# Optimization experiments

Measured on AMD Instinct MI355X. Metric: run time of the kernel, lower is better.

The kernel has to match this reference:

```python
import jax, jax.numpy as jnp
import numpy as np

B, N, C_IN, C_CH = 1, 512, 128, 128

def layer_norm(x, g, b, eps=1e-5):
    mu = jnp.mean(x, axis=-1, keepdims=True)
    var = jnp.var(x, axis=-1, keepdims=True)
    return (x - mu) * jax.lax.rsqrt(var + eps) * g + b

def setup_inputs() -> dict:
    key = jax.random.key(0)
    ks = jax.random.split(key, 16)
    s = 0.02
    # weights stored as [in, out] (torch Linear uses y = x @ W.T + b; we pre-transpose)
    return {
        "z": jax.random.normal(ks[0], (B, N, N, C_IN), jnp.float32),
        "mask": jax.random.randint(ks[1], (B, N, N), 0, 2).astype(bool),
        "g_in": jnp.ones((C_IN,), jnp.float32),
        "b_in": jnp.zeros((C_IN,), jnp.float32),
        "Wa": jax.random.normal(ks[2], (C_IN, C_CH), jnp.float32) * s,
        "ba": jnp.zeros((C_CH,), jnp.float32),
        "Wga": jax.random.normal(ks[3], (C_IN, C_CH), jnp.float32) * s,
        "bga": jax.random.normal(ks[4], (C_CH,), jnp.float32) * s,
        "Wb": jax.random.normal(ks[5], (C_IN, C_CH), jnp.float32) * s,
        "bb": jnp.zeros((C_CH,), jnp.float32),
        "Wgb": jax.random.normal(ks[6], (C_IN, C_CH), jnp.float32) * s,
        "bgb": jax.random.normal(ks[7], (C_CH,), jnp.float32) * s,
        "g_o": jnp.ones((C_CH,), jnp.float32),
        "b_o": jnp.zeros((C_CH,), jnp.float32),
        "Wgo": jax.random.normal(ks[8], (C_IN, C_IN), jnp.float32) * s,
        "bgo": jax.random.normal(ks[9], (C_IN,), jnp.float32) * s,
        "Wo": jax.random.normal(ks[10], (C_CH, C_IN), jnp.float32) * s,
        "bo": jnp.zeros((C_IN,), jnp.float32),
    }

def reference(z, mask, g_in, b_in, Wa, ba, Wga, bga, Wb, bb, Wgb, bgb,
              g_o, b_o, Wgo, bgo, Wo, bo):
    zn = layer_norm(z, g_in, b_in)                                  # [B,N,N,Cin]
    a = jax.nn.sigmoid(zn @ Wga + bga) * (zn @ Wa + ba)             # [B,N,N,Cch]
    b = jax.nn.sigmoid(zn @ Wgb + bgb) * (zn @ Wb + bb)
    m = mask[..., None]                                             # [B,N,N,1]
    a = jnp.where(m, 0.0, a)
    b = jnp.where(m, 0.0, b)
    # axis == 1: k[b,i,j,o] = sum_k a[b,i,k,o] * b[b,j,k,o]
    k = jnp.einsum('biko,bjko->bijo', a, b)
    return jax.nn.sigmoid(zn @ Wgo + bgo) * (layer_norm(k, g_o, b_o) @ Wo + bo)
```

## Files before the change

### kernel.cpp

```cpp
#include <hip/hip_runtime.h>

#define NDIM 512
#define CDIM 128
#define RDIM (NDIM * NDIM)

typedef __attribute__((ext_vector_type(8))) short bf16x8;
typedef __attribute__((ext_vector_type(8))) unsigned short ushort8;
typedef __attribute__((ext_vector_type(4))) float f32x4;

__device__ __forceinline__ float bf2f(unsigned short u) {
  union { unsigned int i; float f; } v; v.i = ((unsigned int)u) << 16; return v.f;
}
__device__ __forceinline__ unsigned short f2bf(float f) {
  union { float f; unsigned int i; } v; v.f = f;
  unsigned int r = v.i + 0x7fffu + ((v.i >> 16) & 1u);
  return (unsigned short)(r >> 16);
}
__device__ __forceinline__ float sigm(float x) { return 1.0f / (1.0f + __expf(-x)); }

__device__ __forceinline__ int sw(int row, int col) {
  return (row << 7) + ((((col >> 3) ^ (row & 7)) << 3) | (col & 7));
}

__global__ __launch_bounds__(256) void k0_prep(
    const float* __restrict__ Wga, const float* __restrict__ Wa,
    const float* __restrict__ Wgb, const float* __restrict__ Wb,
    const float* __restrict__ Wgo, const float* __restrict__ Wo,
    unsigned short* __restrict__ wsT, unsigned short* __restrict__ wsF) {
  __shared__ unsigned short T[128 * 130];
  const float* src;
  switch (blockIdx.x) {
    case 0: src = Wga; break;
    case 1: src = Wa;  break;
    case 2: src = Wgb; break;
    case 3: src = Wb;  break;
    case 4: src = Wgo; break;
    default: src = Wo; break;
  }
  const int t = threadIdx.x;
  unsigned short* dstT = wsT + blockIdx.x * (CDIM * CDIM);
  const int r = t >> 1, hf = t & 1;
  const float* s = src + r * CDIM + hf * 64;
  for (int i = 0; i < 64; i++) T[r * 130 + hf * 64 + i] = f2bf(s[i]);
  __syncthreads();
  unsigned short* d = dstT + r * CDIM + hf * 64;
  for (int i = 0; i < 64; i++) d[i] = T[(hf * 64 + i) * 130 + r];
  unsigned short* dstF = wsF + blockIdx.x * 16384;
  for (int gid = t; gid < 2048; gid += 256) {
    const int fragid = gid >> 6, lane = gid & 63;
    const int kc = fragid >> 3, nf = fragid & 7;
    const int o = nf * 16 + (lane & 15);
    const int c0 = kc * 32 + (lane >> 4) * 8;
#pragma unroll
    for (int j = 0; j < 8; j++) dstF[gid * 8 + j] = f2bf(src[(c0 + j) * CDIM + o]);
  }
}

__device__ __forceinline__ bf16x8 ldfrag(const unsigned short* wf, int slot, int kc,
                                         int nf, int lane) {
  return *((const bf16x8*)(wf + (((slot * 32 + kc * 8 + nf) * 64 + lane) << 3)));
}

__global__ __launch_bounds__(256, 3) void k1_proj(
    const float* __restrict__ z, const int* __restrict__ mask,
    const float* __restrict__ g_in, const float* __restrict__ b_in,
    const float* __restrict__ bga, const float* __restrict__ ba,
    const float* __restrict__ bgb, const float* __restrict__ bb,
    const float* __restrict__ bgo, const unsigned short* __restrict__ wf,
    unsigned short* __restrict__ a_t, unsigned short* __restrict__ b_t,
    float* __restrict__ gate_out) {
  __shared__ unsigned short Xs[CDIM * CDIM];
  const int t = threadIdx.x;
  const int lane = t & 63;
  const int w = t >> 6;
  const int l15 = lane & 15, lq = lane >> 4;
  const int row0 = blockIdx.x * 128;

  {
    const int row = t >> 1, hf = t & 1;
    const float4* zp = (const float4*)(z + (size_t)(row0 + row) * CDIM + hf * 64);
    float s = 0.f, s2 = 0.f;
#pragma unroll
    for (int i = 0; i < 16; i++) {
      float4 x = zp[i];
      s += x.x + x.y + x.z + x.w;
      s2 += x.x * x.x + x.y * x.y + x.z * x.z + x.w * x.w;
    }
    s += __shfl_xor(s, 1);
    s2 += __shfl_xor(s2, 1);
    const float mean = s * 0.0078125f;
    const float var = s2 * 0.0078125f - mean * mean;
    const float rs = rsqrtf(var + 1e-5f);
    const float4* gp = (const float4*)(g_in + hf * 64);
    const float4* bp = (const float4*)(b_in + hf * 64);
#pragma unroll 4
    for (int u = 0; u < 8; u++) {
      float4 x0 = zp[2 * u], x1 = zp[2 * u + 1];
      float4 g0 = gp[2 * u], g1 = gp[2 * u + 1];
      float4 c0 = bp[2 * u], c1 = bp[2 * u + 1];
      ushort8 pk;
      pk[0] = f2bf((x0.x - mean) * rs * g0.x + c0.x);
      pk[1] = f2bf((x0.y - mean) * rs * g0.y + c0.y);
      pk[2] = f2bf((x0.z - mean) * rs * g0.z + c0.z);
      pk[3] = f2bf((x0.w - mean) * rs * g0.w + c0.w);
      pk[4] = f2bf((x1.x - mean) * rs * g1.x + c1.x);
      pk[5] = f2bf((x1.y - mean) * rs * g1.y + c1.y);
      pk[6] = f2bf((x1.z - mean) * rs * g1.z + c1.z);
      pk[7] = f2bf((x1.w - mean) * rs * g1.w + c1.w);
      const int su = (hf * 8 + u) ^ (row & 7);
      *((ushort8*)&Xs[(row << 7) + (su << 3)]) = pk;
    }
  }

  unsigned mbits = 0;
#pragma unroll
  for (int ms = 0; ms < 2; ms++)
#pragma unroll
    for (int r = 0; r < 4; r++) {
      const int rl = w * 32 + ms * 16 + (lq << 2) + r;
      if (mask[row0 + rl] != 0) mbits |= 1u << (ms * 4 + r);
    }

  __syncthreads();

  bf16x8 afr[2][4];
#pragma unroll
  for (int ms = 0; ms < 2; ms++) {
    const int m = w * 32 + ms * 16 + l15;
#pragma unroll
    for (int kc = 0; kc < 4; kc++)
      afr[ms][kc] = *((const bf16x8*)&Xs[sw(m, kc * 32 + (lq << 3))]);
  }
  __syncthreads();

  const f32x4 zv = {0.f, 0.f, 0.f, 0.f};

#pragma unroll 1
  for (int pair = 0; pair < 2; pair++) {
    const int sg = pair * 2, sv = pair * 2 + 1;
    const float* bgp = (pair == 0) ? bga : bgb;
    const float* bvp = (pair == 0) ? ba : bb;
#pragma unroll 1
    for (int half = 0; half < 2; half++) {
      f32x4 accg[2][4], accv[2][4];
#pragma unroll
      for (int i = 0; i < 2; i++)
#pragma unroll
        for (int j = 0; j < 4; j++) { accg[i][j] = zv; accv[i][j] = zv; }
#pragma unroll
      for (int kc = 0; kc < 4; kc++) {
#pragma unroll
        for (int nfh = 0; nfh < 4; nfh++) {
          const int fi = half * 4 + nfh;
          bf16x8 bg = ldfrag(wf, sg, kc, fi, lane);
          bf16x8 bv = ldfrag(wf, sv, kc, fi, lane);
          accg[0][nfh] = __builtin_amdgcn_mfma_f32_16x16x32_bf16(afr[0][kc], bg, accg[0][nfh], 0, 0, 0);
          accg[1][nfh] = __builtin_amdgcn_mfma_f32_16x16x32_bf16(afr[1][kc], bg, accg[1][nfh], 0, 0, 0);
          accv[0][nfh] = __builtin_amdgcn_mfma_f32_16x16x32_bf16(afr[0][kc], bv, accv[0][nfh], 0, 0, 0);
          accv[1][nfh] = __builtin_amdgcn_mfma_f32_16x16x32_bf16(afr[1][kc], bv, accv[1][nfh], 0, 0, 0);
        }
      }
#pragma unroll
      for (int ms = 0; ms < 2; ms++)
#pragma unroll
        for (int nfh = 0; nfh < 4; nfh++) {
          const int n = half * 64 + nfh * 16 + l15;
          const float bg = bgp[n], bv = bvp[n];
#pragma unroll
          for (int r = 0; r < 4; r++) {
            const int rl = w * 32 + ms * 16 + (lq << 2) + r;
            float val = sigm(accg[ms][nfh][r] + bg) * (accv[ms][nfh][r] + bv);
            if ((mbits >> (ms * 4 + r)) & 1u) val = 0.f;
            Xs[sw(n, rl)] = f2bf(val);
          }
        }
    }
    __syncthreads();
    unsigned short* dst = (pair == 0) ? a_t : b_t;
    {
      const int o = t >> 1, hf = t & 1;
#pragma unroll
      for (int u = 0; u < 8; u++) {
        const int ru = hf * 8 + u;
        const int su = ru ^ (o & 7);
        uint4 val = *((const uint4*)&Xs[(o << 7) + (su << 3)]);
        *((uint4*)&dst[(size_t)o * RDIM + row0 + ru * 8]) = val;
      }
    }
    __syncthreads();
  }

#pragma unroll 1
  for (int half = 0; half < 2; half++) {
    f32x4 accg[2][4];
#pragma unroll
    for (int i = 0; i < 2; i++)
#pragma unroll
      for (int j = 0; j < 4; j++) accg[i][j] = zv;
#pragma unroll
    for (int kc = 0; kc < 4; kc++) {
#pragma unroll
      for (int nfh = 0; nfh < 4; nfh++) {
        bf16x8 bg = ldfrag(wf, 4, kc, half * 4 + nfh, lane);
        accg[0][nfh] = __builtin_amdgcn_mfma_f32_16x16x32_bf16(afr[0][kc], bg, accg[0][nfh], 0, 0, 0);
        accg[1][nfh] = __builtin_amdgcn_mfma_f32_16x16x32_bf16(afr[1][kc], bg, accg[1][nfh], 0, 0, 0);
      }
    }
#pragma unroll
    for (int ms = 0; ms < 2; ms++)
#pragma unroll
      for (int nfh = 0; nfh < 4; nfh++) {
        const int n = half * 64 + nfh * 16 + l15;
        const float bg = bgo[n];
#pragma unroll
        for (int r = 0; r < 4; r++) {
          const int rl = w * 32 + ms * 16 + (lq << 2) + r;
          gate_out[(size_t)(row0 + rl) * CDIM + n] = sigm(accg[ms][nfh][r] + bg);
        }
      }
  }
}

__global__ __launch_bounds__(256) void k2_einsum(
    const unsigned short* __restrict__ a_t, const unsigned short* __restrict__ b_t,
    unsigned short* __restrict__ k_t) {
  __shared__ unsigned short As[128 * 72];
  __shared__ unsigned short Bs[128 * 72];
  const int t = threadIdx.x;
  const int lane = t & 63;
  const int w = t >> 6;
  const int l15 = lane & 15, lq = lane >> 4;
  const int o = blockIdx.x >> 4;
  const int tile = blockIdx.x & 15;
  const int i0 = (tile >> 2) * 128, j0 = (tile & 3) * 128;
  const size_t base = (size_t)o * RDIM;

  f32x4 acc[2][8];
  const f32x4 zv = {0.f, 0.f, 0.f, 0.f};
#pragma unroll
  for (int i = 0; i < 2; i++)
#pragma unroll
    for (int j = 0; j < 8; j++) acc[i][j] = zv;

  const int r = t & 127;
  const int isB = t >> 7;
  const unsigned short* srcp = (isB ? b_t : a_t) + base + (size_t)((isB ? j0 : i0) + r) * NDIM;
  unsigned short* dstp = isB ? &Bs[r * 72] : &As[r * 72];

  for (int k0 = 0; k0 < NDIM; k0 += 64) {
    __syncthreads();
    const uint4* s4 = (const uint4*)(srcp + k0);
#pragma unroll
    for (int u = 0; u < 8; u++) *((uint4*)&dstp[u * 8]) = s4[u];
    __syncthreads();
#pragma unroll
    for (int kc = 0; kc < 2; kc++) {
      const int kk = kc * 32 + (lq << 3);
      bf16x8 a0 = *((const bf16x8*)&As[(w * 32 + l15) * 72 + kk]);
      bf16x8 a1 = *((const bf16x8*)&As[(w * 32 + 16 + l15) * 72 + kk]);
#pragma unroll
      for (int nf = 0; nf < 8; nf++) {
        bf16x8 bfr = *((const bf16x8*)&Bs[(nf * 16 + l15) * 72 + kk]);
        acc[0][nf] = __builtin_amdgcn_mfma_f32_16x16x32_bf16(a0, bfr, acc[0][nf], 0, 0, 0);
        acc[1][nf] = __builtin_amdgcn_mfma_f32_16x16x32_bf16(a1, bfr, acc[1][nf], 0, 0, 0);
      }
    }
  }
#pragma unroll
  for (int ms = 0; ms < 2; ms++)
#pragma unroll
    for (int nf = 0; nf < 8; nf++)
#pragma unroll
      for (int r2 = 0; r2 < 4; r2++) {
        const int mi = i0 + w * 32 + ms * 16 + (lq << 2) + r2;
        const int nj = j0 + nf * 16 + l15;
        k_t[base + (size_t)mi * NDIM + nj] = f2bf(acc[ms][nf][r2]);
      }
}

__global__ __launch_bounds__(256) void k3_final(
    const unsigned short* __restrict__ k_t, const unsigned short* __restrict__ wsW,
    const float* __restrict__ g_o, const float* __restrict__ b_o,
    const float* __restrict__ bo, float* __restrict__ out) {
  __shared__ unsigned short Ks[CDIM * CDIM];
  __shared__ unsigned short XN[CDIM * CDIM];
  const int t = threadIdx.x;
  const int lane = t & 63;
  const int w = t >> 6;
  const int l15 = lane & 15, lq = lane >> 4;
  const int row0 = blockIdx.x * 128;

  {
    const int o = t >> 1, hf = t & 1;
    const uint4* src = (const uint4*)(k_t + (size_t)o * RDIM + row0 + hf * 64);
#pragma unroll
    for (int u = 0; u < 8; u++) {
      const int ru = hf * 8 + u;
      const int su = ru ^ (o & 7);
      *((uint4*)&Ks[(o << 7) + (su << 3)]) = src[u];
    }
  }
  __syncthreads();
  {
    const int row = t >> 1, hf = t & 1;
    float x[64];
    float s = 0.f, s2 = 0.f;
#pragma unroll
    for (int i = 0; i < 64; i++) {
      x[i] = bf2f(Ks[sw(hf * 64 + i, row)]);
      s += x[i];
      s2 += x[i] * x[i];
    }
    s += __shfl_xor(s, 1);
    s2 += __shfl_xor(s2, 1);
    const float mean = s * 0.0078125f;
    const float var = s2 * 0.0078125f - mean * mean;
    const float rs = rsqrtf(var + 1e-5f);
#pragma unroll
    for (int i = 0; i < 64; i++) {
      const int o = hf * 64 + i;
      XN[sw(row, o)] = f2bf((x[i] - mean) * rs * g_o[o] + b_o[o]);
    }
  }
  __syncthreads();
  {
    const unsigned short* Wg = wsW + 5 * (CDIM * CDIM);
    const int o = t >> 1, hf = t & 1;
    const uint4* src = (const uint4*)(Wg + o * CDIM + hf * 64);
#pragma unroll
    for (int u = 0; u < 8; u++) {
      const int su = (hf * 8 + u) ^ (o & 7);
      *((uint4*)&Ks[(o << 7) + (su << 3)]) = src[u];
    }
  }
  __syncthreads();

  f32x4 acc[2][8];
  const f32x4 zv = {0.f, 0.f, 0.f, 0.f};
#pragma unroll
  for (int i = 0; i < 2; i++)
#pragma unroll
    for (int j = 0; j < 8; j++) acc[i][j] = zv;

  bf16x8 afr[2][4];
#pragma unroll
  for (int ms = 0; ms < 2; ms++) {
    const int m = w * 32 + ms * 16 + l15;
#pragma unroll
    for (int kc = 0; kc < 4; kc++)
      afr[ms][kc] = *((const bf16x8*)&XN[sw(m, kc * 32 + (lq << 3))]);
  }
#pragma unroll
  for (int kc = 0; kc < 4; kc++) {
    const int kk = kc * 32 + (lq << 3);
#pragma unroll
    for (int nf = 0; nf < 8; nf++) {
      bf16x8 bfr = *((const bf16x8*)&Ks[sw(nf * 16 + l15, kk)]);
      acc[0][nf] = __builtin_amdgcn_mfma_f32_16x16x32_bf16(afr[0][kc], bfr, acc[0][nf], 0, 0, 0);
      acc[1][nf] = __builtin_amdgcn_mfma_f32_16x16x32_bf16(afr[1][kc], bfr, acc[1][nf], 0, 0, 0);
    }
  }
#pragma unroll
  for (int ms = 0; ms < 2; ms++)
#pragma unroll
    for (int nf = 0; nf < 8; nf++) {
      const int n = nf * 16 + l15;
      const float bn = bo[n];
#pragma unroll
      for (int r = 0; r < 4; r++) {
        const int rl = w * 32 + ms * 16 + (lq << 2) + r;
        const size_t idx = (size_t)(row0 + rl) * CDIM + n;
        out[idx] = out[idx] * (acc[ms][nf][r] + bn);
      }
    }
}

extern "C" void kernel_launch(void* const* d_in, const int* in_sizes, int n_in,
                              void* d_out, int out_size, void* d_ws, size_t ws_size,
                              hipStream_t stream) {
  const float* z    = (const float*)d_in[0];
  const int*   mask = (const int*)d_in[1];
  const float* g_in = (const float*)d_in[2];
  const float* b_in = (const float*)d_in[3];
  const float* Wa   = (const float*)d_in[4];
  const float* ba   = (const float*)d_in[5];
  const float* Wga  = (const float*)d_in[6];
  const float* bga  = (const float*)d_in[7];
  const float* Wb   = (const float*)d_in[8];
  const float* bb   = (const float*)d_in[9];
  const float* Wgb  = (const float*)d_in[10];
  const float* bgb  = (const float*)d_in[11];
  const float* g_o  = (const float*)d_in[12];
  const float* b_o  = (const float*)d_in[13];
  const float* Wgo  = (const float*)d_in[14];
  const float* bgo  = (const float*)d_in[15];
  const float* Wo   = (const float*)d_in[16];
  const float* bo   = (const float*)d_in[17];
  float* out = (float*)d_out;

  unsigned short* wsT = (unsigned short*)d_ws;
  unsigned short* wsF = wsT + 6 * (CDIM * CDIM);
  unsigned short* a_t = wsF + 6 * (CDIM * CDIM);
  unsigned short* b_t = a_t + (size_t)CDIM * RDIM;
  unsigned short* k_t = b_t + (size_t)CDIM * RDIM;

  k0_prep<<<6, 256, 0, stream>>>(Wga, Wa, Wgb, Wb, Wgo, Wo, wsT, wsF);
  k1_proj<<<RDIM / 128, 256, 0, stream>>>(z, mask, g_in, b_in, bga, ba, bgb, bb,
                                          bgo, wsF, a_t, b_t, out);
  k2_einsum<<<CDIM * 16, 256, 0, stream>>>(a_t, b_t, k_t);
  k3_final<<<RDIM / 128, 256, 0, stream>>>(k_t, wsT, g_o, b_o, bo, out);
}
```

Measured before the change: 673.8 us.

## Move output gate projection into final kernel and remix einsum block order

The sigmoid(zn@Wgo) gate is no longer computed in the projection kernel and written as fp32 to the output buffer. The final kernel now recomputes the input layernorm from z and computes the gate and Wo projections together from pre-fragmented weights, writing the output once. This drops the transposed weight copy and the fp32 read-modify-write of the output. The cost is re-reading z (128 MB fp32) in the final kernel. The einsum block index is also permuted to interleave channels across blocks, and the final kernel gets a launch_bounds occupancy hint.

```diff
diff --git a/kernel.cpp b/kernel.cpp
--- a/kernel.cpp
+++ b/kernel.cpp
@@ -26,8 +26,7 @@
     const float* __restrict__ Wga, const float* __restrict__ Wa,
     const float* __restrict__ Wgb, const float* __restrict__ Wb,
     const float* __restrict__ Wgo, const float* __restrict__ Wo,
-    unsigned short* __restrict__ wsT, unsigned short* __restrict__ wsF) {
-  __shared__ unsigned short T[128 * 130];
+    unsigned short* __restrict__ wsF) {
   const float* src;
   switch (blockIdx.x) {
     case 0: src = Wga; break;
@@ -38,13 +37,6 @@
     default: src = Wo; break;
   }
   const int t = threadIdx.x;
-  unsigned short* dstT = wsT + blockIdx.x * (CDIM * CDIM);
-  const int r = t >> 1, hf = t & 1;
-  const float* s = src + r * CDIM + hf * 64;
-  for (int i = 0; i < 64; i++) T[r * 130 + hf * 64 + i] = f2bf(s[i]);
-  __syncthreads();
-  unsigned short* d = dstT + r * CDIM + hf * 64;
-  for (int i = 0; i < 64; i++) d[i] = T[(hf * 64 + i) * 130 + r];
   unsigned short* dstF = wsF + blockIdx.x * 16384;
   for (int gid = t; gid < 2048; gid += 256) {
     const int fragid = gid >> 6, lane = gid & 63;
@@ -66,9 +58,8 @@
     const float* __restrict__ g_in, const float* __restrict__ b_in,
     const float* __restrict__ bga, const float* __restrict__ ba,
     const float* __restrict__ bgb, const float* __restrict__ bb,
-    const float* __restrict__ bgo, const unsigned short* __restrict__ wf,
-    unsigned short* __restrict__ a_t, unsigned short* __restrict__ b_t,
-    float* __restrict__ gate_out) {
+    const unsigned short* __restrict__ wf,
+    unsigned short* __restrict__ a_t, unsigned short* __restrict__ b_t) {
   __shared__ unsigned short Xs[CDIM * CDIM];
   const int t = threadIdx.x;
   const int lane = t & 63;
@@ -189,36 +180,6 @@
     }
     __syncthreads();
   }
-
-#pragma unroll 1
-  for (int half = 0; half < 2; half++) {
-    f32x4 accg[2][4];
-#pragma unroll
-    for (int i = 0; i < 2; i++)
-#pragma unroll
-      for (int j = 0; j < 4; j++) accg[i][j] = zv;
-#pragma unroll
-    for (int kc = 0; kc < 4; kc++) {
-#pragma unroll
-      for (int nfh = 0; nfh < 4; nfh++) {
-        bf16x8 bg = ldfrag(wf, 4, kc, half * 4 + nfh, lane);
-        accg[0][nfh] = __builtin_amdgcn_mfma_f32_16x16x32_bf16(afr[0][kc], bg, accg[0][nfh], 0, 0, 0);
-        accg[1][nfh] = __builtin_amdgcn_mfma_f32_16x16x32_bf16(afr[1][kc], bg, accg[1][nfh], 0, 0, 0);
-      }
-    }
-#pragma unroll
-    for (int ms = 0; ms < 2; ms++)
-#pragma unroll
-      for (int nfh = 0; nfh < 4; nfh++) {
-        const int n = half * 64 + nfh * 16 + l15;
-        const float bg = bgo[n];
-#pragma unroll
-        for (int r = 0; r < 4; r++) {
-          const int rl = w * 32 + ms * 16 + (lq << 2) + r;
-          gate_out[(size_t)(row0 + rl) * CDIM + n] = sigm(accg[ms][nfh][r] + bg);
-        }
-      }
-  }
 }
 
 __global__ __launch_bounds__(256) void k2_einsum(
@@ -230,8 +191,9 @@
   const int lane = t & 63;
   const int w = t >> 6;
   const int l15 = lane & 15, lq = lane >> 4;
-  const int o = blockIdx.x >> 4;
-  const int tile = blockIdx.x & 15;
+  const int bid = (blockIdx.x & 7) * (2048 >> 3) + (blockIdx.x >> 3);
+  const int o = bid >> 4;
+  const int tile = bid & 15;
   const int i0 = (tile >> 2) * 128, j0 = (tile & 3) * 128;
   const size_t base = (size_t)o * RDIM;
 
@@ -278,9 +240,11 @@
       }
 }
 
-__global__ __launch_bounds__(256) void k3_final(
-    const unsigned short* __restrict__ k_t, const unsigned short* __restrict__ wsW,
-    const float* __restrict__ g_o, const float* __restrict__ b_o,
+__global__ __launch_bounds__(256, 2) void k3_final(
+    const unsigned short* __restrict__ k_t, const unsigned short* __restrict__ wf,
+    const float* __restrict__ z, const float* __restrict__ g_in,
+    const float* __restrict__ b_in, const float* __restrict__ g_o,
+    const float* __restrict__ b_o, const float* __restrict__ bgo,
     const float* __restrict__ bo, float* __restrict__ out) {
   __shared__ unsigned short Ks[CDIM * CDIM];
   __shared__ unsigned short XN[CDIM * CDIM];
@@ -300,22 +264,68 @@
       *((uint4*)&Ks[(o << 7) + (su << 3)]) = src[u];
     }
   }
-  __syncthreads();
   {
     const int row = t >> 1, hf = t & 1;
-    float x[64];
+    const float4* zp = (const float4*)(z + (size_t)(row0 + row) * CDIM + hf * 64);
     float s = 0.f, s2 = 0.f;
 #pragma unroll
-    for (int i = 0; i < 64; i++) {
-      x[i] = bf2f(Ks[sw(hf * 64 + i, row)]);
-      s += x[i];
-      s2 += x[i] * x[i];
+    for (int i = 0; i < 16; i++) {
+      float4 x = zp[i];
+      s += x.x + x.y + x.z + x.w;
+      s2 += x.x * x.x + x.y * x.y + x.z * x.z + x.w * x.w;
     }
     s += __shfl_xor(s, 1);
     s2 += __shfl_xor(s2, 1);
     const float mean = s * 0.0078125f;
     const float var = s2 * 0.0078125f - mean * mean;
     const float rs = rsqrtf(var + 1e-5f);
+    const float4* gp = (const float4*)(g_in + hf * 64);
+    const float4* bp = (const float4*)(b_in + hf * 64);
+#pragma unroll 4
+    for (int u = 0; u < 8; u++) {
+      float4 x0 = zp[2 * u], x1 = zp[2 * u + 1];
+      float4 g0 = gp[2 * u], g1 = gp[2 * u + 1];
+      float4 c0 = bp[2 * u], c1 = bp[2 * u + 1];
+      ushort8 pk;
+      pk[0] = f2bf((x0.x - mean) * rs * g0.x + c0.x);
+      pk[1] = f2bf((x0.y - mean) * rs * g0.y + c0.y);
+      pk[2] = f2bf((x0.z - mean) * rs * g0.z + c0.z);
+      pk[3] = f2bf((x0.w - mean) * rs * g0.w + c0.w);
+      pk[4] = f2bf((x1.x - mean) * rs * g1.x + c1.x);
+      pk[5] = f2bf((x1.y - mean) * rs * g1.y + c1.y);
+      pk[6] = f2bf((x1.z - mean) * rs * g1.z + c1.z);
+      pk[7] = f2bf((x1.w - mean) * rs * g1.w + c1.w);
+      const int su = (hf * 8 + u) ^ (row & 7);
+      *((ushort8*)&XN[(row << 7) + (su << 3)]) = pk;
+    }
+  }
+  __syncthreads();
+
+  bf16x8 az[2][4];
+#pragma unroll
+  for (int ms = 0; ms < 2; ms++) {
+    const int m = w * 32 + ms * 16 + l15;
+#pragma unroll
+    for (int kc = 0; kc < 4; kc++)
+      az[ms][kc] = *((const bf16x8*)&XN[sw(m, kc * 32 + (lq << 3))]);
+  }
+  __syncthreads();
+
+  {
+    const int row = t >> 1, hf = t & 1;
+    float x[64];
+    float s = 0.f, s2 = 0.f;
+#pragma unroll
+    for (int i = 0; i < 64; i++) {
+      x[i] = bf2f(Ks[sw(hf * 64 + i, row)]);
+      s += x[i];
+      s2 += x[i] * x[i];
+    }
+    s += __shfl_xor(s, 1);
+    s2 += __shfl_xor(s2, 1);
+    const float mean = s * 0.0078125f;
+    const float var = s2 * 0.0078125f - mean * mean;
+    const float rs = rsqrtf(var + 1e-5f);
 #pragma unroll
     for (int i = 0; i < 64; i++) {
       const int o = hf * 64 + i;
@@ -323,56 +333,51 @@
     }
   }
   __syncthreads();
-  {
-    const unsigned short* Wg = wsW + 5 * (CDIM * CDIM);
-    const int o = t >> 1, hf = t & 1;
-    const uint4* src = (const uint4*)(Wg + o * CDIM + hf * 64);
-#pragma unroll
-    for (int u = 0; u < 8; u++) {
-      const int su = (hf * 8 + u) ^ (o & 7);
-      *((uint4*)&Ks[(o << 7) + (su << 3)]) = src[u];
-    }
-  }
-  __syncthreads();
-
-  f32x4 acc[2][8];
-  const f32x4 zv = {0.f, 0.f, 0.f, 0.f};
-#pragma unroll
-  for (int i = 0; i < 2; i++)
-#pragma unroll
-    for (int j = 0; j < 8; j++) acc[i][j] = zv;
-
-  bf16x8 afr[2][4];
+
+  bf16x8 ak[2][4];
 #pragma unroll
   for (int ms = 0; ms < 2; ms++) {
     const int m = w * 32 + ms * 16 + l15;
 #pragma unroll
     for (int kc = 0; kc < 4; kc++)
-      afr[ms][kc] = *((const bf16x8*)&XN[sw(m, kc * 32 + (lq << 3))]);
-  }
-#pragma unroll
-  for (int kc = 0; kc < 4; kc++) {
-    const int kk = kc * 32 + (lq << 3);
-#pragma unroll
-    for (int nf = 0; nf < 8; nf++) {
-      bf16x8 bfr = *((const bf16x8*)&Ks[sw(nf * 16 + l15, kk)]);
-      acc[0][nf] = __builtin_amdgcn_mfma_f32_16x16x32_bf16(afr[0][kc], bfr, acc[0][nf], 0, 0, 0);
-      acc[1][nf] = __builtin_amdgcn_mfma_f32_16x16x32_bf16(afr[1][kc], bfr, acc[1][nf], 0, 0, 0);
-    }
-  }
-#pragma unroll
-  for (int ms = 0; ms < 2; ms++)
-#pragma unroll
-    for (int nf = 0; nf < 8; nf++) {
-      const int n = nf * 16 + l15;
-      const float bn = bo[n];
-#pragma unroll
-      for (int r = 0; r < 4; r++) {
-        const int rl = w * 32 + ms * 16 + (lq << 2) + r;
-        const size_t idx = (size_t)(row0 + rl) * CDIM + n;
-        out[idx] = out[idx] * (acc[ms][nf][r] + bn);
-      }
-    }
+      ak[ms][kc] = *((const bf16x8*)&XN[sw(m, kc * 32 + (lq << 3))]);
+  }
+
+  const f32x4 zv = {0.f, 0.f, 0.f, 0.f};
+#pragma unroll 1
+  for (int half = 0; half < 2; half++) {
+    f32x4 accg[2][4], acco[2][4];
+#pragma unroll
+    for (int i = 0; i < 2; i++)
+#pragma unroll
+      for (int j = 0; j < 4; j++) { accg[i][j] = zv; acco[i][j] = zv; }
+#pragma unroll
+    for (int kc = 0; kc < 4; kc++) {
+#pragma unroll
+      for (int nfh = 0; nfh < 4; nfh++) {
+        const int fi = half * 4 + nfh;
+        bf16x8 bg = ldfrag(wf, 4, kc, fi, lane);
+        bf16x8 bw = ldfrag(wf, 5, kc, fi, lane);
+        accg[0][nfh] = __builtin_amdgcn_mfma_f32_16x16x32_bf16(az[0][kc], bg, accg[0][nfh], 0, 0, 0);
+        accg[1][nfh] = __builtin_amdgcn_mfma_f32_16x16x32_bf16(az[1][kc], bg, accg[1][nfh], 0, 0, 0);
+        acco[0][nfh] = __builtin_amdgcn_mfma_f32_16x16x32_bf16(ak[0][kc], bw, acco[0][nfh], 0, 0, 0);
+        acco[1][nfh] = __builtin_amdgcn_mfma_f32_16x16x32_bf16(ak[1][kc], bw, acco[1][nfh], 0, 0, 0);
+      }
+    }
+#pragma unroll
+    for (int ms = 0; ms < 2; ms++)
+#pragma unroll
+      for (int nfh = 0; nfh < 4; nfh++) {
+        const int n = half * 64 + nfh * 16 + l15;
+        const float gb = bgo[n], ob = bo[n];
+#pragma unroll
+        for (int r = 0; r < 4; r++) {
+          const int rl = w * 32 + ms * 16 + (lq << 2) + r;
+          out[(size_t)(row0 + rl) * CDIM + n] =
+              sigm(accg[ms][nfh][r] + gb) * (acco[ms][nfh][r] + ob);
+        }
+      }
+  }
 }
 
 extern "C" void kernel_launch(void* const* d_in, const int* in_sizes, int n_in,
@@ -398,15 +403,15 @@
   const float* bo   = (const float*)d_in[17];
   float* out = (float*)d_out;
 
-  unsigned short* wsT = (unsigned short*)d_ws;
-  unsigned short* wsF = wsT + 6 * (CDIM * CDIM);
+  unsigned short* wsF = (unsigned short*)d_ws;
   unsigned short* a_t = wsF + 6 * (CDIM * CDIM);
   unsigned short* b_t = a_t + (size_t)CDIM * RDIM;
   unsigned short* k_t = b_t + (size_t)CDIM * RDIM;
 
-  k0_prep<<<6, 256, 0, stream>>>(Wga, Wa, Wgb, Wb, Wgo, Wo, wsT, wsF);
+  k0_prep<<<6, 256, 0, stream>>>(Wga, Wa, Wgb, Wb, Wgo, Wo, wsF);
   k1_proj<<<RDIM / 128, 256, 0, stream>>>(z, mask, g_in, b_in, bga, ba, bgb, bb,
-                                          bgo, wsF, a_t, b_t, out);
+                                          wsF, a_t, b_t);
   k2_einsum<<<CDIM * 16, 256, 0, stream>>>(a_t, b_t, k_t);
-  k3_final<<<RDIM / 128, 256, 0, stream>>>(k_t, wsT, g_o, b_o, bo, out);
-}
+  k3_final<<<RDIM / 128, 256, 0, stream>>>(k_t, wsF, z, g_in, b_in, g_o, b_o,
+                                           bgo, bo, out);
+}
```

Result: no change. 666.2 us (-1.1%).
